# Kernel tuning notes

Measured on AMD Instinct MI355X. Metric: run time of the kernel, lower is better.

Reference implementation:

```python
import jax, jax.numpy as jnp
import numpy as np


def _rel_shift(x):
    # Transformer-XL relative shift. x: [batch, heads, qlen, klen]
    b, n, i, j = x.shape
    x = jnp.pad(x, ((0, 0), (0, 0), (0, 0), (1, 0)))  # zero-pad along key axis
    x = x.reshape(b, n, j + 1, i)[:, :, 1:, :]
    return x.reshape(b, n, i, j)


def setup_inputs() -> dict:
    key = jax.random.key(0)
    ks = jax.random.split(key, 7)
    QLEN, B, D, H, DH = 2048, 4, 1024, 16, 64
    DO = H * DH
    s = 1.0 / np.sqrt(D)
    return {
        "word_embed": jax.random.normal(ks[0], (QLEN, B, D), jnp.float32),
        "pos_embed": jax.random.normal(ks[1], (QLEN, D), jnp.float32),
        "bias_q": jax.random.normal(ks[2], (H, DH), jnp.float32) * 0.02,
        "bias_k": jax.random.normal(ks[3], (H, DH), jnp.float32) * 0.02,
        "W_qkv": jax.random.normal(ks[4], (D, 3 * DO), jnp.float32) * s,
        "W_r": jax.random.normal(ks[5], (D, DO), jnp.float32) * s,
        "b_r": jnp.zeros((DO,), jnp.float32),
    }


def reference(word_embed, pos_embed, bias_q, bias_k, W_qkv, W_r, b_r):
    qlen, bsz, dim = word_embed.shape
    H, Dh = bias_q.shape
    plen = pos_embed.shape[0]

    # fused QKV projection (no bias, as in torch Linear(bias=False))
    qkv = jnp.einsum('ibd,de->ibe', word_embed, W_qkv)  # [qlen, b, 3*H*Dh]
    q, k, v = jnp.split(qkv, 3, axis=-1)
    q = q.reshape(qlen, bsz, H, Dh)
    k = k.reshape(qlen, bsz, H, Dh)
    v = v.reshape(qlen, bsz, H, Dh)

    # positional projection (r_net has bias)
    r = (pos_embed @ W_r + b_r).reshape(plen, H, Dh)  # [plen, H, Dh]

    # content (AC) and position (BD) score terms
    AC = jnp.einsum('ibnd,jbnd->bnij', q + bias_q, k)   # [b, H, qlen, klen]
    BD = jnp.einsum('ibnd,jnd->bnij', q + bias_k, r)    # [b, H, qlen, plen]
    BD = _rel_shift(BD)

    scale = float(Dh) ** 0.5
    attn = jax.nn.softmax((AC + BD) / scale, axis=-1)
    ctx = jnp.einsum('bnij,jbnd->ibnd', attn, v)        # [qlen, b, H, Dh]
    return ctx.reshape(qlen, bsz, H * Dh)
```

## Files before the change

kernel.cpp:

```cpp
#include <hip/hip_runtime.h>
#include <stdint.h>

typedef unsigned short u16;
typedef __attribute__((ext_vector_type(8))) short  s16x8;
typedef __attribute__((ext_vector_type(8))) __bf16 b16x8;
typedef __attribute__((ext_vector_type(4))) float  f32x4;

__device__ __forceinline__ float bf2f(u16 u){
  union { unsigned int ui; float f; } v; v.ui = ((unsigned int)u) << 16; return v.f;
}
__device__ __forceinline__ u16 f2bf(float f){
  union { float f; unsigned int ui; } v; v.f = f;
  unsigned int u = v.ui;
  u += 0x7FFFu + ((u >> 16) & 1u);
  return (u16)(u >> 16);
}
__device__ __forceinline__ f32x4 mfma16(s16x8 a, s16x8 b, f32x4 c){
  return __builtin_amdgcn_mfma_f32_16x16x32_bf16(
      __builtin_bit_cast(b16x8, a), __builtin_bit_cast(b16x8, b), c, 0, 0, 0);
}
__device__ __forceinline__ void gload_lds16(const u16* g, u16* l){
  __builtin_amdgcn_global_load_lds(
      (const __attribute__((address_space(1))) unsigned int*)(g),
      (__attribute__((address_space(3))) unsigned int*)(l), 16, 0, 0);
}
__device__ __forceinline__ uint32_t cvt_pk_bf16(float lo, float hi){
  uint32_t r;
  asm("v_cvt_pk_bf16_f32 %0, %1, %2" : "=v"(r) : "v"(lo), "v"(hi));
  return r;
}

__global__ __launch_bounds__(256) void cast_f32_bf16(const float* __restrict__ in,
                                                     u16* __restrict__ out, int n8){
  int i = blockIdx.x * 256 + threadIdx.x;
  if (i >= n8) return;
  const f32x4* p = (const f32x4*)(in + (size_t)i * 8);
  f32x4 a = p[0], c = p[1];
  s16x8 o;
#pragma unroll
  for (int j = 0; j < 4; j++){ o[j] = (short)f2bf(a[j]); o[j+4] = (short)f2bf(c[j]); }
  *(s16x8*)(out + (size_t)i * 8) = o;
}

__global__ __launch_bounds__(256) void tcast(const float* __restrict__ in,
                                             u16* __restrict__ out, int R, int C){
  __shared__ float tile[32][33];
  int c0 = blockIdx.x * 32, r0 = blockIdx.y * 32;
  int tc = threadIdx.x & 31, tr = threadIdx.x >> 5;
#pragma unroll
  for (int p = 0; p < 4; p++)
    tile[tr + 8*p][tc] = in[(size_t)(r0 + tr + 8*p) * C + c0 + tc];
  __syncthreads();
  int rr = threadIdx.x & 31, cc = threadIdx.x >> 5;
#pragma unroll
  for (int p = 0; p < 4; p++)
    out[(size_t)(c0 + cc + 8*p) * R + r0 + rr] = f2bf(tile[rr][cc + 8*p]);
}

__global__ __launch_bounds__(256) void gemm_bt(const u16* __restrict__ A,
                                               const u16* __restrict__ Bt,
                                               int mode,
                                               u16* __restrict__ Qo, u16* __restrict__ Ko,
                                               u16* __restrict__ Vo, u16* __restrict__ Ro,
                                               const float* __restrict__ brp){
  __shared__ __align__(16) u16 lsA[2][128 * 32];
  __shared__ __align__(16) u16 lsB[2][128 * 32];
  int m0 = blockIdx.y * 128, n0 = blockIdx.x * 128;
  int t = threadIdx.x, wid = t >> 6, lane = t & 63;
  int lrow = lane & 15, lk = lane >> 4;
  int wr = wid >> 1, wc = wid & 1;

  f32x4 acc[4][4];
#pragma unroll
  for (int i = 0; i < 4; i++)
#pragma unroll
    for (int j = 0; j < 4; j++) acc[i][j] = (f32x4){0.f, 0.f, 0.f, 0.f};

  const u16* Ab = A  + (size_t)m0 * 1024;
  const u16* Bb = Bt + (size_t)n0 * 1024;

  s16x8 ra[2], rb[2];
#pragma unroll
  for (int p = 0; p < 2; p++){
    int c = p * 256 + t;
    ra[p] = *(const s16x8*)(Ab + (size_t)(c >> 2) * 1024 + (c & 3) * 8);
    rb[p] = *(const s16x8*)(Bb + (size_t)(c >> 2) * 1024 + (c & 3) * 8);
  }

  for (int kt = 0; kt < 32; kt++){
    int buf = kt & 1;
#pragma unroll
    for (int p = 0; p < 2; p++){
      int c = p * 256 + t;
      *(s16x8*)(lsA[buf] + (size_t)c * 8) = ra[p];
      *(s16x8*)(lsB[buf] + (size_t)c * 8) = rb[p];
    }
    __syncthreads();
    if (kt < 31){
      int k0 = (kt + 1) * 32;
#pragma unroll
      for (int p = 0; p < 2; p++){
        int c = p * 256 + t;
        ra[p] = *(const s16x8*)(Ab + (size_t)(c >> 2) * 1024 + k0 + (c & 3) * 8);
        rb[p] = *(const s16x8*)(Bb + (size_t)(c >> 2) * 1024 + k0 + (c & 3) * 8);
      }
    }
    s16x8 af[4], bfr[4];
#pragma unroll
    for (int i = 0; i < 4; i++)
      af[i] = *(const s16x8*)(lsA[buf] + (wr * 64 + i * 16 + lrow) * 32 + lk * 8);
#pragma unroll
    for (int j = 0; j < 4; j++)
      bfr[j] = *(const s16x8*)(lsB[buf] + (wc * 64 + j * 16 + lrow) * 32 + lk * 8);
#pragma unroll
    for (int i = 0; i < 4; i++)
#pragma unroll
      for (int j = 0; j < 4; j++)
        acc[i][j] = mfma16(af[i], bfr[j], acc[i][j]);
    __syncthreads();
  }

#pragma unroll
  for (int i = 0; i < 4; i++)
#pragma unroll
    for (int j = 0; j < 4; j++){
      int mbase = m0 + wr * 64 + i * 16 + lk * 4;
      int ncol  = n0 + wc * 64 + j * 16 + lrow;
#pragma unroll
      for (int r = 0; r < 4; r++){
        int m = mbase + r;
        float val = acc[i][j][r];
        if (mode == 0){
          int sel = ncol >> 10;
          int hd = ncol & 1023;
          int h = hd >> 6, dh = hd & 63;
          int b = m & 3, iq = m >> 2;
          size_t o = ((size_t)(b * 16 + h) * 2048 + iq) * 64 + dh;
          u16 vb = f2bf(val);
          if (sel == 0) Qo[o] = vb; else if (sel == 1) Ko[o] = vb; else Vo[o] = vb;
        } else {
          int h = ncol >> 6, dh = ncol & 63;
          Ro[((size_t)h * 4224 + m) * 64 + dh] = f2bf(val + brp[ncol]);
        }
      }
    }
}

__global__ __launch_bounds__(256) void transpose_v(const u16* __restrict__ V,
                                                   u16* __restrict__ VT){
  __shared__ u16 tile[64][65];
  int bh = blockIdx.y, i0 = blockIdx.x * 64;
  const u16* src = V + ((size_t)bh * 2048 + i0) * 64;
  int t = threadIdx.x;
#pragma unroll
  for (int p = 0; p < 2; p++){
    int idx = (p * 256 + t) * 8;
    int row = idx >> 6, col = idx & 63;
    s16x8 v = *(const s16x8*)(src + idx);
#pragma unroll
    for (int e = 0; e < 8; e++) tile[row][col + e] = (u16)v[e];
  }
  __syncthreads();
  u16* dst = VT + (size_t)bh * 64 * 2048 + i0;
#pragma unroll
  for (int p = 0; p < 2; p++){
    int idx = (p * 256 + t) * 8;
    int dh = idx >> 6, ii = idx & 63;
    s16x8 o;
#pragma unroll
    for (int e = 0; e < 8; e++) o[e] = (short)tile[ii + e][dh];
    *(s16x8*)(dst + (size_t)dh * 2048 + ii) = o;
  }
}

__global__ __launch_bounds__(256) void attn9_kernel(const u16* __restrict__ Qm,
                                                    const u16* __restrict__ Km,
                                                    const u16* __restrict__ Vt,
                                                    const u16* __restrict__ Rm,
                                                    const float* __restrict__ bq,
                                                    const float* __restrict__ bk,
                                                    float* __restrict__ Out){
  __shared__ __align__(16) u16   Kt[2][64 * 64];
  __shared__ __align__(16) u16   Vs[2][64 * 64];
  __shared__ __align__(16) float Gs[4][16 * 84];

  int lin = blockIdx.x;
  int xcd = lin & 7, j = lin >> 3;
  int hb = xcd * 8 + (j >> 5);
  int bx = j & 31;
  int h = hb & 15, b = hb >> 4;

  const int wid = threadIdx.x >> 6, lane = threadIdx.x & 63;
  const int lrow = lane & 15, lk = lane >> 4;
  const int q0 = bx * 64 + wid * 16;
  const size_t bh = (size_t)b * 16 + h;
  const u16* Qp = Qm + bh * 2048 * 64;
  const u16* Kp = Km + bh * 2048 * 64;
  const u16* Vp = Vt + bh * 64 * 2048;
  const u16* Rp = Rm + ((size_t)h * 4224 + 128) * 64;
  float* Gw = Gs[wid];
  u16*   Pw = (u16*)Gs[wid];

  const float cs = 0.125f * 1.44269504088896f;

  s16x8 qa[2], qb0[2], qb1[2];
  {
    const float* bqp = bq + h * 64;
    const float* bkp = bk + h * 64;
    int r1 = q0 + lrow + 1; if (r1 > 2047) r1 = 2047;
#pragma unroll
    for (int d = 0; d < 2; d++){
      int doff = d * 32 + lk * 8;
      s16x8 raw  = *(const s16x8*)(Qp + (size_t)(q0 + lrow) * 64 + doff);
      s16x8 raw1 = *(const s16x8*)(Qp + (size_t)r1 * 64 + doff);
      s16x8 a, c0, c1;
#pragma unroll
      for (int jj = 0; jj < 8; jj++){
        float qv = bf2f((u16)raw[jj]);
        float q1 = bf2f((u16)raw1[jj]);
        a[jj]  = (short)f2bf(cs * (qv + bqp[doff + jj]));
        c0[jj] = (short)f2bf(cs * (qv + bkp[doff + jj]));
        c1[jj] = (short)f2bf(cs * (q1 + bkp[doff + jj]));
      }
      qa[d] = a; qb0[d] = c0; qb1[d] = c1;
    }
  }

  const u16* r1p = Rp + (size_t)(2032 - q0 + lrow) * 64 + lk * 8;
  const u16* r2p = r1p - (size_t)2049 * 64;

  float m = -3.0e38f, l = 0.f;
  f32x4 Oc[4];
#pragma unroll
  for (int f = 0; f < 4; f++) Oc[f] = (f32x4){0.f, 0.f, 0.f, 0.f};

  const int wbase = 15 - lrow + 4 * lk;
  const int dl0   = 4 * lk - lrow;

  {
#pragma unroll
    for (int i = 0; i < 2; i++){
      int g = wid * 2 + i;
      int row = g * 8 + (lane >> 3);
      int sch = (lane & 7) ^ (row & 7);
      gload_lds16(Kp + (size_t)row * 64 + sch * 8, Kt[0] + g * 512);
      gload_lds16(Vp + (size_t)row * 2048 + 0 + sch * 8, Vs[0] + g * 512);
    }
  }
  __syncthreads();

  for (int t = 0; t < 32; t++){
    const int k0 = t * 64;
    const int cur = t & 1;
    const int d0 = k0 - q0;
    const bool n1 = (d0 <= 15);
    const bool n2 = (d0 >= -61);
    const int dlane = d0 + dl0;

    const u16* rp = n1 ? r1p : r2p;
    s16x8 rr[5][2];
#pragma unroll
    for (int wf = 0; wf < 5; wf++){
      rr[wf][0] = *(const s16x8*)(rp + wf * 1024);
      rr[wf][1] = *(const s16x8*)(rp + wf * 1024 + 32);
    }

    if (t < 31){
      const u16* Kn = Kp + (size_t)(k0 + 64) * 64;
#pragma unroll
      for (int i = 0; i < 2; i++){
        int g = wid * 2 + i;
        int row = g * 8 + (lane >> 3);
        int sch = (lane & 7) ^ (row & 7);
        gload_lds16(Kn + (size_t)row * 64 + sch * 8, Kt[cur ^ 1] + g * 512);
        gload_lds16(Vp + (size_t)row * 2048 + (k0 + 64) + sch * 8, Vs[cur ^ 1] + g * 512);
      }
    }

    f32x4 S[4];
    __builtin_amdgcn_s_setprio(1);
#pragma unroll
    for (int kf = 0; kf < 4; kf++){
      f32x4 acc = (f32x4){0.f, 0.f, 0.f, 0.f};
#pragma unroll
      for (int d = 0; d < 2; d++){
        int row = kf * 16 + lrow;
        int ch = (d * 4 + lk) ^ (row & 7);
        s16x8 kfr = *(const s16x8*)(Kt[cur] + row * 64 + ch * 8);
        acc = mfma16(kfr, qa[d], acc);
      }
      S[kf] = acc;
    }
    __builtin_amdgcn_s_setprio(0);

    {
      const s16x8* qs = n1 ? qb0 : qb1;
#pragma unroll
      for (int wf = 0; wf < 5; wf++){
        f32x4 g = (f32x4){0.f, 0.f, 0.f, 0.f};
        g = mfma16(rr[wf][0], qs[0], g);
        g = mfma16(rr[wf][1], qs[1], g);
        *(f32x4*)(Gw + lrow * 84 + wf * 16 + 4 * lk) = g;
      }
      const float* gp = Gw + lrow * 84 + wbase;
      if (n1){
#pragma unroll
        for (int kf = 0; kf < 4; kf++)
#pragma unroll
          for (int r = 0; r < 4; r++){
            float g = gp[kf * 16 + r];
            S[kf][r] += (dlane + kf * 16 + r <= 0) ? g : 0.f;
          }
      } else {
#pragma unroll
        for (int kf = 0; kf < 4; kf++)
#pragma unroll
          for (int r = 0; r < 4; r++){
            float g = gp[kf * 16 + r];
            S[kf][r] += (dlane + kf * 16 + r >= 2) ? g : 0.f;
          }
      }
    }
    if (n1 && n2){
#pragma unroll
      for (int wf = 0; wf < 5; wf++){
        rr[wf][0] = *(const s16x8*)(r2p + wf * 1024);
        rr[wf][1] = *(const s16x8*)(r2p + wf * 1024 + 32);
      }
#pragma unroll
      for (int wf = 0; wf < 5; wf++){
        f32x4 g = (f32x4){0.f, 0.f, 0.f, 0.f};
        g = mfma16(rr[wf][0], qb1[0], g);
        g = mfma16(rr[wf][1], qb1[1], g);
        *(f32x4*)(Gw + lrow * 84 + wf * 16 + 4 * lk) = g;
      }
      const float* gp = Gw + lrow * 84 + wbase;
#pragma unroll
      for (int kf = 0; kf < 4; kf++)
#pragma unroll
        for (int r = 0; r < 4; r++){
          float g = gp[kf * 16 + r];
          S[kf][r] += (dlane + kf * 16 + r >= 2) ? g : 0.f;
        }
    }

    float tmax = -3.0e38f;
#pragma unroll
    for (int kf = 0; kf < 4; kf++)
#pragma unroll
      for (int r = 0; r < 4; r++) tmax = fmaxf(tmax, S[kf][r]);
    tmax = fmaxf(tmax, __shfl_xor(tmax, 16, 64));
    tmax = fmaxf(tmax, __shfl_xor(tmax, 32, 64));
    if (tmax > m + 11.5f){
      float al = exp2f(m - tmax);
      l *= al;
#pragma unroll
      for (int f = 0; f < 4; f++) Oc[f] *= al;
      m = tmax;
    }
    float sum = 0.f;
#pragma unroll
    for (int kf = 0; kf < 4; kf++)
#pragma unroll
      for (int r = 0; r < 4; r++){
        float p = exp2f(S[kf][r] - m);
        S[kf][r] = p;
        sum += p;
      }
    sum += __shfl_xor(sum, 16, 64);
    sum += __shfl_xor(sum, 32, 64);
    l += sum;

#pragma unroll
    for (int kf = 0; kf < 4; kf++){
      uint32_t u0 = cvt_pk_bf16(S[kf][0], S[kf][1]);
      uint32_t u1 = cvt_pk_bf16(S[kf][2], S[kf][3]);
      *(uint32_t*)(Pw + lrow * 88 + kf * 16 + 4 * lk)     = u0;
      *(uint32_t*)(Pw + lrow * 88 + kf * 16 + 4 * lk + 2) = u1;
    }

    __builtin_amdgcn_s_setprio(1);
#pragma unroll
    for (int ks = 0; ks < 2; ks++){
      s16x8 pB = *(const s16x8*)(Pw + lrow * 88 + ks * 32 + lk * 8);
#pragma unroll
      for (int f = 0; f < 4; f++){
        int row = f * 16 + lrow;
        int ch = (ks * 4 + lk) ^ (row & 7);
        s16x8 vfr = *(const s16x8*)(Vs[cur] + row * 64 + ch * 8);
        Oc[f] = mfma16(vfr, pB, Oc[f]);
      }
    }
    __builtin_amdgcn_s_setprio(0);

    r1p += 64 * 64; r2p += 64 * 64;
    __syncthreads();
  }

  float inv = 1.0f / l;
#pragma unroll
  for (int f = 0; f < 4; f++){
    f32x4 o = Oc[f] * inv;
    *(f32x4*)(Out + (size_t)(q0 + lrow) * 4096 + b * 1024 + h * 64 + f * 16 + 4 * lk) = o;
  }
}

extern "C" void kernel_launch(void* const* d_in, const int* in_sizes, int n_in,
                              void* d_out, int out_size, void* d_ws, size_t ws_size,
                              hipStream_t stream){
  const float* word = (const float*)d_in[0];
  const float* pos  = (const float*)d_in[1];
  const float* bq   = (const float*)d_in[2];
  const float* bk   = (const float*)d_in[3];
  const float* Wqkv = (const float*)d_in[4];
  const float* Wr   = (const float*)d_in[5];
  const float* br   = (const float*)d_in[6];
  float* out = (float*)d_out;

  char* ws = (char*)d_ws;
  size_t off = 0;
  u16* Abf   = (u16*)(ws + off); off += (size_t)8192 * 1024 * 2;
  u16* WqkvT = (u16*)(ws + off); off += (size_t)3072 * 1024 * 2;
  u16* Pbf   = (u16*)(ws + off); off += (size_t)2048 * 1024 * 2;
  u16* WrT   = (u16*)(ws + off); off += (size_t)1024 * 1024 * 2;
  u16* Qb    = (u16*)(ws + off); off += (size_t)64 * 2048 * 64 * 2;
  u16* Kb    = (u16*)(ws + off); off += (size_t)64 * 2048 * 64 * 2;
  u16* Vb    = (u16*)(ws + off); off += (size_t)64 * 2048 * 64 * 2;
  u16* VTb   = (u16*)(ws + off); off += (size_t)64 * 64 * 2048 * 2;
  u16* Rb    = (u16*)(ws + off); off += (size_t)16 * 4224 * 64 * 2;
  if (ws_size < off) return;

  cast_f32_bf16<<<4096, 256, 0, stream>>>(word, Abf, 1048576);
  cast_f32_bf16<<<1024, 256, 0, stream>>>(pos,  Pbf, 262144);
  tcast<<<dim3(96, 32), 256, 0, stream>>>(Wqkv, WqkvT, 1024, 3072);
  tcast<<<dim3(32, 32), 256, 0, stream>>>(Wr,   WrT,   1024, 1024);
  gemm_bt<<<dim3(24, 64), 256, 0, stream>>>(Abf, WqkvT, 0, Qb, Kb, Vb, nullptr, nullptr);
  gemm_bt<<<dim3(8, 16),  256, 0, stream>>>(Pbf, WrT, 1, nullptr, nullptr, nullptr,
                                            Rb + (size_t)128 * 64, br);
  transpose_v<<<dim3(32, 64), 256, 0, stream>>>(Vb, VTb);
  attn9_kernel<<<2048, 256, 0, stream>>>(Qb, Kb, VTb, Rb, bq, bk, out);
}
```

Before: 495.8 us.

## Single-buffer K/V tiles, prefetch R after compute, add unmasked fast path

```diff
diff --git a/kernel.cpp b/kernel.cpp
--- a/kernel.cpp
+++ b/kernel.cpp
@@ -173,15 +173,15 @@
   }
 }
 
-__global__ __launch_bounds__(256) void attn9_kernel(const u16* __restrict__ Qm,
-                                                    const u16* __restrict__ Km,
-                                                    const u16* __restrict__ Vt,
-                                                    const u16* __restrict__ Rm,
-                                                    const float* __restrict__ bq,
-                                                    const float* __restrict__ bk,
-                                                    float* __restrict__ Out){
-  __shared__ __align__(16) u16   Kt[2][64 * 64];
-  __shared__ __align__(16) u16   Vs[2][64 * 64];
+__global__ __launch_bounds__(256) void attn12_kernel(const u16* __restrict__ Qm,
+                                                     const u16* __restrict__ Km,
+                                                     const u16* __restrict__ Vt,
+                                                     const u16* __restrict__ Rm,
+                                                     const float* __restrict__ bq,
+                                                     const float* __restrict__ bk,
+                                                     float* __restrict__ Out){
+  __shared__ __align__(16) u16   Kt[64 * 64];
+  __shared__ __align__(16) u16   Vs[64 * 64];
   __shared__ __align__(16) float Gs[4][16 * 84];
 
   int lin = blockIdx.x;
@@ -237,45 +237,29 @@
   const int wbase = 15 - lrow + 4 * lk;
   const int dl0   = 4 * lk - lrow;
 
-  {
-#pragma unroll
-    for (int i = 0; i < 2; i++){
-      int g = wid * 2 + i;
-      int row = g * 8 + (lane >> 3);
-      int sch = (lane & 7) ^ (row & 7);
-      gload_lds16(Kp + (size_t)row * 64 + sch * 8, Kt[0] + g * 512);
-      gload_lds16(Vp + (size_t)row * 2048 + 0 + sch * 8, Vs[0] + g * 512);
-    }
+  s16x8 rr[5][2];
+#pragma unroll
+  for (int wf = 0; wf < 5; wf++){
+    rr[wf][0] = *(const s16x8*)(r1p + wf * 1024);
+    rr[wf][1] = *(const s16x8*)(r1p + wf * 1024 + 32);
+  }
+#pragma unroll
+  for (int i = 0; i < 2; i++){
+    int g = wid * 2 + i;
+    int row = g * 8 + (lane >> 3);
+    int sch = (lane & 7) ^ (row & 7);
+    gload_lds16(Kp + (size_t)row * 64 + sch * 8, Kt + g * 512);
+    gload_lds16(Vp + (size_t)row * 2048 + sch * 8, Vs + g * 512);
   }
   __syncthreads();
 
   for (int t = 0; t < 32; t++){
     const int k0 = t * 64;
-    const int cur = t & 1;
     const int d0 = k0 - q0;
     const bool n1 = (d0 <= 15);
     const bool n2 = (d0 >= -61);
+    const bool pure = (d0 <= -63) | (d0 >= 17);
     const int dlane = d0 + dl0;
-
-    const u16* rp = n1 ? r1p : r2p;
-    s16x8 rr[5][2];
-#pragma unroll
-    for (int wf = 0; wf < 5; wf++){
-      rr[wf][0] = *(const s16x8*)(rp + wf * 1024);
-      rr[wf][1] = *(const s16x8*)(rp + wf * 1024 + 32);
-    }
-
-    if (t < 31){
-      const u16* Kn = Kp + (size_t)(k0 + 64) * 64;
-#pragma unroll
-      for (int i = 0; i < 2; i++){
-        int g = wid * 2 + i;
-        int row = g * 8 + (lane >> 3);
-        int sch = (lane & 7) ^ (row & 7);
-        gload_lds16(Kn + (size_t)row * 64 + sch * 8, Kt[cur ^ 1] + g * 512);
-        gload_lds16(Vp + (size_t)row * 2048 + (k0 + 64) + sch * 8, Vs[cur ^ 1] + g * 512);
-      }
-    }
 
     f32x4 S[4];
     __builtin_amdgcn_s_setprio(1);
@@ -286,7 +270,7 @@
       for (int d = 0; d < 2; d++){
         int row = kf * 16 + lrow;
         int ch = (d * 4 + lk) ^ (row & 7);
-        s16x8 kfr = *(const s16x8*)(Kt[cur] + row * 64 + ch * 8);
+        s16x8 kfr = *(const s16x8*)(Kt + row * 64 + ch * 8);
         acc = mfma16(kfr, qa[d], acc);
       }
       S[kf] = acc;
@@ -303,7 +287,12 @@
         *(f32x4*)(Gw + lrow * 84 + wf * 16 + 4 * lk) = g;
       }
       const float* gp = Gw + lrow * 84 + wbase;
-      if (n1){
+      if (pure){
+#pragma unroll
+        for (int kf = 0; kf < 4; kf++)
+#pragma unroll
+          for (int r = 0; r < 4; r++) S[kf][r] += gp[kf * 16 + r];
+      } else if (n1){
 #pragma unroll
         for (int kf = 0; kf < 4; kf++)
 #pragma unroll
@@ -344,11 +333,11 @@
         }
     }
 
-    float tmax = -3.0e38f;
-#pragma unroll
-    for (int kf = 0; kf < 4; kf++)
-#pragma unroll
-      for (int r = 0; r < 4; r++) tmax = fmaxf(tmax, S[kf][r]);
+    float e0 = fmaxf(fmaxf(S[0][0], S[0][1]), fmaxf(S[0][2], S[0][3]));
+    float e1 = fmaxf(fmaxf(S[1][0], S[1][1]), fmaxf(S[1][2], S[1][3]));
+    float e2 = fmaxf(fmaxf(S[2][0], S[2][1]), fmaxf(S[2][2], S[2][3]));
+    float e3 = fmaxf(fmaxf(S[3][0], S[3][1]), fmaxf(S[3][2], S[3][3]));
+    float tmax = fmaxf(fmaxf(e0, e1), fmaxf(e2, e3));
     tmax = fmaxf(tmax, __shfl_xor(tmax, 16, 64));
     tmax = fmaxf(tmax, __shfl_xor(tmax, 32, 64));
     if (tmax > m + 11.5f){
@@ -358,15 +347,16 @@
       for (int f = 0; f < 4; f++) Oc[f] *= al;
       m = tmax;
     }
-    float sum = 0.f;
 #pragma unroll
     for (int kf = 0; kf < 4; kf++)
 #pragma unroll
-      for (int r = 0; r < 4; r++){
-        float p = exp2f(S[kf][r] - m);
-        S[kf][r] = p;
-        sum += p;
-      }
+      for (int r = 0; r < 4; r++)
+        S[kf][r] = exp2f(S[kf][r] - m);
+    float s0 = (S[0][0] + S[0][1]) + (S[0][2] + S[0][3]);
+    float s1 = (S[1][0] + S[1][1]) + (S[1][2] + S[1][3]);
+    float s2 = (S[2][0] + S[2][1]) + (S[2][2] + S[2][3]);
+    float s3 = (S[3][0] + S[3][1]) + (S[3][2] + S[3][3]);
+    float sum = (s0 + s1) + (s2 + s3);
     sum += __shfl_xor(sum, 16, 64);
     sum += __shfl_xor(sum, 32, 64);
     l += sum;
@@ -387,13 +377,31 @@
       for (int f = 0; f < 4; f++){
         int row = f * 16 + lrow;
         int ch = (ks * 4 + lk) ^ (row & 7);
-        s16x8 vfr = *(const s16x8*)(Vs[cur] + row * 64 + ch * 8);
+        s16x8 vfr = *(const s16x8*)(Vs + row * 64 + ch * 8);
         Oc[f] = mfma16(vfr, pB, Oc[f]);
       }
     }
     __builtin_amdgcn_s_setprio(0);
 
+    __syncthreads();
     r1p += 64 * 64; r2p += 64 * 64;
+    if (t < 31){
+      const u16* Kn = Kp + (size_t)(k0 + 64) * 64;
+#pragma unroll
+      for (int i = 0; i < 2; i++){
+        int g = wid * 2 + i;
+        int row = g * 8 + (lane >> 3);
+        int sch = (lane & 7) ^ (row & 7);
+        gload_lds16(Kn + (size_t)row * 64 + sch * 8, Kt + g * 512);
+        gload_lds16(Vp + (size_t)row * 2048 + (k0 + 64) + sch * 8, Vs + g * 512);
+      }
+      const u16* rp = ((d0 + 64) <= 15) ? r1p : r2p;
+#pragma unroll
+      for (int wf = 0; wf < 5; wf++){
+        rr[wf][0] = *(const s16x8*)(rp + wf * 1024);
+        rr[wf][1] = *(const s16x8*)(rp + wf * 1024 + 32);
+      }
+    }
     __syncthreads();
   }
 
@@ -438,5 +446,5 @@
   gemm_bt<<<dim3(8, 16),  256, 0, stream>>>(Pbf, WrT, 1, nullptr, nullptr, nullptr,
                                             Rb + (size_t)128 * 64, br);
   transpose_v<<<dim3(32, 64), 256, 0, stream>>>(Vb, VTb);
-  attn9_kernel<<<2048, 256, 0, stream>>>(Qb, Kb, VTb, Rb, bq, bk, out);
-}
+  attn12_kernel<<<2048, 256, 0, stream>>>(Qb, Kb, VTb, Rb, bq, bk, out);
+}
```

Result: no change. 495.0 us (-0.2%).
